# Kernel tuning notes

Hardware: AMD Instinct MI355X
Metric: run time of the kernel (lower is better)

The kernel has to match this reference:

```python
import jax, jax.numpy as jnp
from jax import lax
import numpy as np

BN_EPS = 1e-5

def nearest_resize(x, out_h, out_w):
    # torch F.interpolate(mode='nearest'): src = floor(dst * in / out)
    B, C, H, W = x.shape
    hi = (jnp.arange(out_h) * H) // out_h
    wi = (jnp.arange(out_w) * W) // out_w
    return x[:, :, hi][:, :, :, wi]

def conv1x1(x, w, b=None):
    y = jnp.einsum('bchw,oc->bohw', x, w)
    if b is not None:
        y = y + b[None, :, None, None]
    return y

def dwconv(x, w, stride, pad):
    C = x.shape[1]
    return lax.conv_general_dilated(x, w, (stride, stride), [(pad, pad), (pad, pad)],
                                    dimension_numbers=('NCHW', 'OIHW', 'NCHW'),
                                    feature_group_count=C)

def bn(x, g, b, m, v):
    scale = g / jnp.sqrt(v + BN_EPS)
    return (x - m[None, :, None, None]) * scale[None, :, None, None] + b[None, :, None, None]


def setup_inputs() -> dict:
    key = jax.random.key(0)
    ks = jax.random.split(key, 8)
    B, C, H0, W0 = 4, 512, 192, 192
    w_scale = 0.05
    return {
        'x': jax.random.normal(ks[0], (B, C, H0, W0), jnp.float32),
        'q_w': jax.random.normal(ks[1], (C, C), jnp.float32) * w_scale,
        'q_b': jnp.zeros((C,), jnp.float32),
        'kv_w': jax.random.normal(ks[2], (2 * C, C), jnp.float32) * w_scale,
        'kv_b': jnp.zeros((2 * C,), jnp.float32),
        'sr1_w': jax.random.normal(ks[3], (C, 1, 2, 2), jnp.float32) * w_scale,
        'bn1_g': jnp.ones((C,), jnp.float32),
        'bn1_b': jnp.zeros((C,), jnp.float32),
        'bn1_m': jnp.zeros((C,), jnp.float32),
        'bn1_v': jnp.ones((C,), jnp.float32),
        'sr2_w': jax.random.normal(ks[4], (C, C), jnp.float32) * w_scale,
        'bn2_g': jnp.ones((C,), jnp.float32),
        'bn2_b': jnp.zeros((C,), jnp.float32),
        'bn2_m': jnp.zeros((C,), jnp.float32),
        'bn2_v': jnp.ones((C,), jnp.float32),
        'lc_w': jax.random.normal(ks[5], (C, 1, 3, 3), jnp.float32) * w_scale,
        'lc_b': jnp.zeros((C,), jnp.float32),
        'head_num': 8,
    }


def reference(x, q_w, q_b, kv_w, kv_b, sr1_w, bn1_g, bn1_b, bn1_m, bn1_v,
              sr2_w, bn2_g, bn2_b, bn2_m, bn2_v, lc_w, lc_b, head_num):
    origin_h, origin_w = x.shape[2], x.shape[3]
    x = nearest_resize(x, origin_h // 4, origin_w // 4)
    B, C, H, W = x.shape
    hd = C // head_num
    scale = hd ** (-0.5)

    # q projection (1x1 conv with bias)
    q = conv1x1(x, q_w, q_b)  # [B,C,H,W]

    # spatial reduction: depthwise conv(k=sr, s=sr, p=sr//2) + BN + ReLU, then 1x1 + BN
    sr = sr1_w.shape[-1]
    kv = jax.nn.relu(bn(dwconv(x, sr1_w, sr, sr // 2), bn1_g, bn1_b, bn1_m, bn1_v))
    kv = bn(conv1x1(kv, sr2_w), bn2_g, bn2_b, bn2_m, bn2_v)

    # local depthwise 3x3 conv residual
    kv = dwconv(kv, lc_w, 1, 1) + lc_b[None, :, None, None] + kv

    # kv projection (1x1 conv, 2C output)
    kv = conv1x1(kv, kv_w, kv_b)
    k, v = jnp.split(kv, 2, axis=1)  # each [B,C,Hs,Ws]
    M = k.shape[2] * k.shape[3]

    q_ = jnp.swapaxes(q.reshape(B, head_num, hd, H * W), -1, -2)  # [B,h,N,hd]
    k_ = k.reshape(B, head_num, hd, M)                             # [B,h,hd,M]
    v_ = jnp.swapaxes(v.reshape(B, head_num, hd, M), -1, -2)       # [B,h,M,hd]

    attn = jax.nn.softmax(jnp.matmul(q_, k_) * scale, axis=-1)     # [B,h,N,M]
    out = jnp.swapaxes(jnp.matmul(attn, v_), -1, -2).reshape(B, C, H, W)

    # NOTE: original torch code passes size=(origin_w, origin_h)
    out = nearest_resize(out, origin_w, origin_h)
    return out
```

## Files before the change

### kernel.cpp

```cpp
#include <hip/hip_runtime.h>

#define Bsz 4
#define Cc  512
#define C2  1024
#define H0c 192
#define Hh  48
#define Nn  2304
#define HNh 8
#define HD  64
#define Hs  25
#define Ms  625

typedef const float* fp;
typedef _Float16 f16;
typedef __attribute__((ext_vector_type(8))) _Float16 f16x8;
typedef __attribute__((ext_vector_type(4))) _Float16 f16x4;
typedef __attribute__((ext_vector_type(4))) float    f32x4;

__global__ __launch_bounds__(256) void k_ds_t(fp __restrict__ x,
                                              float* __restrict__ xds,
                                              f16* __restrict__ xt) {
    __shared__ float tile[32][33];
    const int b = blockIdx.z;
    const int s0 = blockIdx.x * 32, r0 = blockIdx.y * 32;
    const int t = threadIdx.x;
    const float* xb = x + (size_t)b * Cc * H0c * H0c;
    float* xdsb = xds + (size_t)b * Cc * Nn;
    #pragma unroll
    for (int p = 0; p < 4; p++) {
        int e = t + p * 256; int i = e >> 5, j = e & 31;
        int c = r0 + i, n = s0 + j;
        float v = xb[((size_t)c * H0c + (n / Hh) * 4) * H0c + (n % Hh) * 4];
        tile[i][j] = v;
        xdsb[(size_t)c * Nn + n] = v;
    }
    __syncthreads();
    #pragma unroll
    for (int p = 0; p < 4; p++) {
        int e = t + p * 256; int oi = e >> 5, oj = e & 31;
        xt[((size_t)b * Nn + s0 + oi) * Cc + r0 + oj] = (f16)tile[oj][oi];
    }
}

__global__ __launch_bounds__(256) void k_sr1t(const float* __restrict__ xds,
                                              fp __restrict__ w, fp g, fp bb, fp bm, fp bv,
                                              f16* __restrict__ kv1t) {
    __shared__ float tile[32][33];
    const int b = blockIdx.z;
    const int s0 = blockIdx.x * 32, r0 = blockIdx.y * 32;
    const int t = threadIdx.x;
    #pragma unroll
    for (int p = 0; p < 4; p++) {
        int e = t + p * 256; int i = e >> 5, j = e & 31;
        int c = r0 + i, n = s0 + j;
        float v = 0.f;
        if (n < Ms) {
            int ho = n / Hs, wo = n % Hs;
            const float* src = xds + ((size_t)b * Cc + c) * Nn;
            float acc = 0.f;
            #pragma unroll
            for (int di = 0; di < 2; di++) {
                int ih = ho * 2 - 1 + di;
                if (ih < 0 || ih >= Hh) continue;
                #pragma unroll
                for (int dj = 0; dj < 2; dj++) {
                    int iw = wo * 2 - 1 + dj;
                    if (iw < 0 || iw >= Hh) continue;
                    acc += w[c * 4 + di * 2 + dj] * src[ih * Hh + iw];
                }
            }
            float sc = g[c] * rsqrtf(bv[c] + 1e-5f);
            v = fmaxf((acc - bm[c]) * sc + bb[c], 0.f);
        }
        tile[i][j] = v;
    }
    __syncthreads();
    #pragma unroll
    for (int p = 0; p < 4; p++) {
        int e = t + p * 256; int oi = e >> 5, oj = e & 31;
        if (s0 + oi < Ms)
            kv1t[((size_t)b * Ms + s0 + oi) * Cc + r0 + oj] = (f16)tile[oj][oi];
    }
}

__global__ __launch_bounds__(256) void k_lct(const float* __restrict__ kv2,
                                             fp __restrict__ w, fp __restrict__ lb,
                                             f16* __restrict__ kv3t) {
    __shared__ float tile[32][33];
    const int b = blockIdx.z;
    const int s0 = blockIdx.x * 32, r0 = blockIdx.y * 32;
    const int t = threadIdx.x;
    #pragma unroll
    for (int p = 0; p < 4; p++) {
        int e = t + p * 256; int i = e >> 5, j = e & 31;
        int c = r0 + i, n = s0 + j;
        float v = 0.f;
        if (n < Ms) {
            int ho = n / Hs, wo = n % Hs;
            const float* src = kv2 + ((size_t)b * Cc + c) * Ms;
            float acc = 0.f;
            #pragma unroll
            for (int di = 0; di < 3; di++) {
                int ih = ho - 1 + di;
                if (ih < 0 || ih >= Hs) continue;
                #pragma unroll
                for (int dj = 0; dj < 3; dj++) {
                    int iw = wo - 1 + dj;
                    if (iw < 0 || iw >= Hs) continue;
                    acc += w[c * 9 + di * 3 + dj] * src[ih * Hs + iw];
                }
            }
            v = acc + lb[c] + src[n];
        }
        tile[i][j] = v;
    }
    __syncthreads();
    #pragma unroll
    for (int p = 0; p < 4; p++) {
        int e = t + p * 256; int oi = e >> 5, oj = e & 31;
        if (s0 + oi < Ms)
            kv3t[((size_t)b * Ms + s0 + oi) * Cc + r0 + oj] = (f16)tile[oj][oi];
    }
}

__global__ __launch_bounds__(256) void k_gemm_mfma(
    const float* __restrict__ W, const f16* __restrict__ Xt,
    float* __restrict__ Yf, f16* __restrict__ Yt, f16* __restrict__ Vt,
    const int Md, const int Nd, const int NtRows, const int mode,
    fp __restrict__ bias,
    fp __restrict__ bn_g, fp __restrict__ bn_b, fp __restrict__ bn_m, fp __restrict__ bn_v)
{
    __shared__ f16 sA[128 * 80];
    __shared__ f16 sB[128 * 80];
    const int b  = blockIdx.z;
    const int m0 = blockIdx.y * 128, n0 = blockIdx.x * 128;
    const int t = threadIdx.x;
    const int lane = t & 63, w = t >> 6;
    const int lm = lane & 15, q = lane >> 4;
    const int wm = w >> 1, wn = w & 1;
    const f16* Xb = Xt + (size_t)b * Nd * 512;

    f32x4 acc[4][4];
    #pragma unroll
    for (int i = 0; i < 4; i++)
        #pragma unroll
        for (int j = 0; j < 4; j++)
            #pragma unroll
            for (int r = 0; r < 4; r++) acc[i][j][r] = 0.f;

    for (int k0 = 0; k0 < 512; k0 += 64) {
        {
            int r = t >> 1, hh = (t & 1) * 32;
            const float* wr = W + (size_t)(m0 + r) * 512 + k0 + hh;
            f16* dst = &sA[r * 80 + hh];
            #pragma unroll
            for (int i = 0; i < 8; i++) {
                float4 v = *(const float4*)&wr[i * 4];
                f16x4 h4; h4[0] = (f16)v.x; h4[1] = (f16)v.y; h4[2] = (f16)v.z; h4[3] = (f16)v.w;
                *(f16x4*)&dst[i * 4] = h4;
            }
        }
        {
            int r = t >> 1, hh = (t & 1) * 32;
            bool ok = (n0 + r) < Nd;
            const f16* xr = Xb + (size_t)(n0 + r) * 512 + k0 + hh;
            f16* dst = &sB[r * 80 + hh];
            #pragma unroll
            for (int i = 0; i < 4; i++) {
                f16x8 v;
                if (ok) {
                    v = *(const f16x8*)&xr[i * 8];
                } else {
                    for (int z = 0; z < 8; z++) v[z] = (f16)0.f;
                }
                *(f16x8*)&dst[i * 8] = v;
            }
        }
        __syncthreads();
        #pragma unroll
        for (int ks = 0; ks < 2; ks++) {
            f16x8 af[4], bf[4];
            #pragma unroll
            for (int i = 0; i < 4; i++)
                af[i] = *(const f16x8*)&sA[(wm * 64 + i * 16 + lm) * 80 + ks * 32 + q * 8];
            #pragma unroll
            for (int j = 0; j < 4; j++)
                bf[j] = *(const f16x8*)&sB[(wn * 64 + j * 16 + lm) * 80 + ks * 32 + q * 8];
            #pragma unroll
            for (int i = 0; i < 4; i++)
                #pragma unroll
                for (int j = 0; j < 4; j++)
                    acc[i][j] = __builtin_amdgcn_mfma_f32_16x16x32_f16(af[i], bf[j], acc[i][j], 0, 0, 0);
        }
        __syncthreads();
    }

    #pragma unroll
    for (int i = 0; i < 4; i++) {
        int ob = m0 + wm * 64 + i * 16 + q * 4;
        float badd[4], bsc[4], bsh[4];
        #pragma unroll
        for (int r = 0; r < 4; r++) {
            int o = ob + r;
            badd[r] = bias ? bias[o] : 0.f;
            if (bn_g) { bsc[r] = bn_g[o] * rsqrtf(bn_v[o] + 1e-5f); bsh[r] = bn_b[o] - bn_m[o] * bsc[r]; }
            else      { bsc[r] = 1.f; bsh[r] = 0.f; }
        }
        #pragma unroll
        for (int j = 0; j < 4; j++) {
            int n = n0 + wn * 64 + j * 16 + lm;
            f32x4 a = acc[i][j];
            if (mode == 0) {
                if (n < Nd) {
                    #pragma unroll
                    for (int r = 0; r < 4; r++)
                        Yf[((size_t)b * Md + ob + r) * Nd + n] = (a[r] + badd[r]) * bsc[r] + bsh[r];
                }
            } else if (mode == 1 || (mode == 2 && ob < 512)) {
                f16x4 h;
                #pragma unroll
                for (int r = 0; r < 4; r++) h[r] = (f16)(a[r] + badd[r]);
                int hh = ob >> 6, d0 = ob & 63;
                *(f16x4*)&Yt[((size_t)(b * 8 + hh) * NtRows + n) * 64 + d0] = h;
            } else {
                #pragma unroll
                for (int r = 0; r < 4; r++) {
                    float val = (n < Nd) ? (a[r] + badd[r]) : 0.f;
                    Vt[((size_t)b * Cc + (ob + r - 512)) * 640 + n] = (f16)val;
                }
            }
        }
    }
}

__global__ __launch_bounds__(256) void k_attn_mfma(
    const f16* __restrict__ Qt, const f16* __restrict__ Kt,
    const f16* __restrict__ Vt, float* __restrict__ out)
{
    __shared__ f16 sK[64 * 80];
    __shared__ f16 sV[64 * 80];
    __shared__ f16 sP[4][16 * 80];

    int bh = blockIdx.y;
    int n0 = blockIdx.x * 64;
    int t = threadIdx.x, w = t >> 6, lane = t & 63;
    int lm = lane & 15, q = lane >> 4;
    f16* sPw = &sP[w][0];

    f16x8 qf[2];
    {
        const f16* qrow = Qt + ((size_t)bh * Nn + n0 + w * 16 + lm) * 64;
        qf[0] = *(const f16x8*)&qrow[q * 8];
        qf[1] = *(const f16x8*)&qrow[32 + q * 8];
    }

    f32x4 od[4];
    #pragma unroll
    for (int dt = 0; dt < 4; dt++)
        #pragma unroll
        for (int r = 0; r < 4; r++) od[dt][r] = 0.f;
    float mold[4], lold[4];
    #pragma unroll
    for (int r = 0; r < 4; r++) { mold[r] = -1e30f; lold[r] = 0.f; }

    int kr = t >> 2, kc = t & 3;
    const f16* kbase = Kt + (size_t)bh * 640 * 64;
    const f16* vbase = Vt + (size_t)bh * 64 * 640;

    for (int mc = 0; mc < 640; mc += 64) {
        {
            const f16* ksrc = kbase + (size_t)(mc + kr) * 64;
            *(f16x8*)&sK[kr * 80 + kc * 8]      = *(const f16x8*)&ksrc[kc * 8];
            *(f16x8*)&sK[kr * 80 + 32 + kc * 8] = *(const f16x8*)&ksrc[32 + kc * 8];
            const f16* vsrc = vbase + (size_t)kr * 640 + mc;
            *(f16x8*)&sV[kr * 80 + kc * 8]      = *(const f16x8*)&vsrc[kc * 8];
            *(f16x8*)&sV[kr * 80 + 32 + kc * 8] = *(const f16x8*)&vsrc[32 + kc * 8];
        }
        __syncthreads();

        f32x4 sc4[4];
        #pragma unroll
        for (int j = 0; j < 4; j++)
            #pragma unroll
            for (int r = 0; r < 4; r++) sc4[j][r] = 0.f;
        #pragma unroll
        for (int ks = 0; ks < 2; ks++) {
            #pragma unroll
            for (int j = 0; j < 4; j++) {
                f16x8 kf = *(const f16x8*)&sK[(j * 16 + lm) * 80 + ks * 32 + q * 8];
                sc4[j] = __builtin_amdgcn_mfma_f32_16x16x32_f16(qf[ks], kf, sc4[j], 0, 0, 0);
            }
        }

        #pragma unroll
        for (int reg = 0; reg < 4; reg++) {
            float mx = -1e30f;
            #pragma unroll
            for (int j = 0; j < 4; j++) {
                float s = sc4[j][reg] * 0.125f;
                if (mc + j * 16 + lm >= Ms) s = -1e30f;
                sc4[j][reg] = s;
                mx = fmaxf(mx, s);
            }
            #pragma unroll
            for (int off = 1; off < 16; off <<= 1) mx = fmaxf(mx, __shfl_xor(mx, off));
            float mnew = fmaxf(mold[reg], mx);
            float alpha = __expf(mold[reg] - mnew);
            float rs = 0.f;
            #pragma unroll
            for (int j = 0; j < 4; j++) {
                float p = __expf(sc4[j][reg] - mnew);
                sc4[j][reg] = p;
                rs += p;
            }
            #pragma unroll
            for (int off = 1; off < 16; off <<= 1) rs += __shfl_xor(rs, off);
            lold[reg] = lold[reg] * alpha + rs;
            mold[reg] = mnew;
            #pragma unroll
            for (int dt = 0; dt < 4; dt++) od[dt][reg] *= alpha;
            #pragma unroll
            for (int j = 0; j < 4; j++)
                sPw[(q * 4 + reg) * 80 + j * 16 + lm] = (f16)sc4[j][reg];
        }

        #pragma unroll
        for (int ks = 0; ks < 2; ks++) {
            f16x8 pa = *(const f16x8*)&sPw[lm * 80 + ks * 32 + q * 8];
            #pragma unroll
            for (int dt = 0; dt < 4; dt++) {
                f16x8 vf = *(const f16x8*)&sV[(dt * 16 + lm) * 80 + ks * 32 + q * 8];
                od[dt] = __builtin_amdgcn_mfma_f32_16x16x32_f16(pa, vf, od[dt], 0, 0, 0);
            }
        }
        __syncthreads();
    }

    float inv4[4];
    #pragma unroll
    for (int r = 0; r < 4; r++) inv4[r] = 1.f / lold[r];
    const int bq = bh >> 3, hch = (bh & 7) * 64;
    const int nq = n0 + w * 16 + q * 4;
    const int i4 = (nq / Hh) * 4, j4 = (nq % Hh) * 4;
    #pragma unroll
    for (int dt = 0; dt < 4; dt++) {
        float* oc = out + ((size_t)(bq * Cc + hch + dt * 16 + lm) * H0c + i4) * H0c + j4;
        #pragma unroll
        for (int r = 0; r < 4; r++) {
            float val = od[dt][r] * inv4[r];
            float4 pk = make_float4(val, val, val, val);
            #pragma unroll
            for (int ii = 0; ii < 4; ii++)
                *(float4*)&oc[ii * H0c + r * 4] = pk;
        }
    }
}

extern "C" void kernel_launch(void* const* d_in, const int* in_sizes, int n_in,
                              void* d_out, int out_size, void* d_ws, size_t ws_size,
                              hipStream_t stream) {
    (void)in_sizes; (void)n_in; (void)out_size; (void)ws_size;
    fp x     = (fp)d_in[0];
    fp q_w   = (fp)d_in[1];
    fp q_b   = (fp)d_in[2];
    fp kv_w  = (fp)d_in[3];
    fp kv_b  = (fp)d_in[4];
    fp sr1_w = (fp)d_in[5];
    fp bn1_g = (fp)d_in[6];
    fp bn1_b = (fp)d_in[7];
    fp bn1_m = (fp)d_in[8];
    fp bn1_v = (fp)d_in[9];
    fp sr2_w = (fp)d_in[10];
    fp bn2_g = (fp)d_in[11];
    fp bn2_b = (fp)d_in[12];
    fp bn2_m = (fp)d_in[13];
    fp bn2_v = (fp)d_in[14];
    fp lc_w  = (fp)d_in[15];
    fp lc_b  = (fp)d_in[16];
    float* out = (float*)d_out;

    float* ws   = (float*)d_ws;
    float* xds  = ws;
    float* kv2  = ws;
    f16*   Kt   = (f16*)(ws + 1310720);
    f16*   vt   = (f16*)(ws + 1966080);
    f16*   xt   = (f16*)(ws + 4718592);
    f16*   kv1t = (f16*)(ws + 4718592);
    f16*   kv3t = (f16*)(ws + 5358592);
    f16*   Qt   = (f16*)(ws + 7077888);

    k_ds_t<<<dim3(72, 16, Bsz), 256, 0, stream>>>(x, xds, xt);
    k_gemm_mfma<<<dim3(18, 4, Bsz), 256, 0, stream>>>(q_w, xt, nullptr, Qt, nullptr,
        Cc, Nn, Nn, 1, q_b, nullptr, nullptr, nullptr, nullptr);
    k_sr1t<<<dim3(20, 16, Bsz), 256, 0, stream>>>(xds, sr1_w, bn1_g, bn1_b, bn1_m, bn1_v, kv1t);
    k_gemm_mfma<<<dim3(5, 4, Bsz), 256, 0, stream>>>(sr2_w, kv1t, kv2, nullptr, nullptr,
        Cc, Ms, 0, 0, nullptr, bn2_g, bn2_b, bn2_m, bn2_v);
    k_lct<<<dim3(20, 16, Bsz), 256, 0, stream>>>(kv2, lc_w, lc_b, kv3t);
    k_gemm_mfma<<<dim3(5, 8, Bsz), 256, 0, stream>>>(kv_w, kv3t, nullptr, Kt, vt,
        C2, Ms, 640, 2, kv_b, nullptr, nullptr, nullptr, nullptr);
    k_attn_mfma<<<dim3(Nn / 64, Bsz * HNh), 256, 0, stream>>>(Qt, Kt, vt, out);
}
```

Before: 690.5 us.

## Pre-convert weights to fp16, fold softmax scale into Q, split upsample into separate kernel

Adds a kernel that converts all three 1x1 weight matrices to fp16 once, so the GEMM loads fp16 weights directly instead of converting fp32 in every tile. The softmax scale is folded into the Q projection epilogue, and masking in attention is limited to the last key chunk. The attention kernel now writes a compact [B*C, N] buffer, and a new coalesced upsample kernel expands it to the full-resolution output. This replaces the strided 16x replicated stores from the attention epilogue, at the cost of extra launches and an extra intermediate round trip through memory.

```diff
diff --git a/kernel.cpp b/kernel.cpp
--- a/kernel.cpp
+++ b/kernel.cpp
@@ -17,6 +17,16 @@
 typedef __attribute__((ext_vector_type(4))) _Float16 f16x4;
 typedef __attribute__((ext_vector_type(4))) float    f32x4;
 
+__global__ __launch_bounds__(256) void k_cvtw(fp __restrict__ q_w, fp __restrict__ sr2_w,
+                                              fp __restrict__ kv_w, f16* __restrict__ wh) {
+    int idx = blockIdx.x * 256 + threadIdx.x;
+    float v;
+    if (idx < 262144)      v = q_w[idx];
+    else if (idx < 524288) v = sr2_w[idx - 262144];
+    else                   v = kv_w[idx - 524288];
+    wh[idx] = (f16)v;
+}
+
 __global__ __launch_bounds__(256) void k_ds_t(fp __restrict__ x,
                                               float* __restrict__ xds,
                                               f16* __restrict__ xt) {
@@ -124,9 +134,9 @@
 }
 
 __global__ __launch_bounds__(256) void k_gemm_mfma(
-    const float* __restrict__ W, const f16* __restrict__ Xt,
+    const f16* __restrict__ W, const f16* __restrict__ Xt,
     float* __restrict__ Yf, f16* __restrict__ Yt, f16* __restrict__ Vt,
-    const int Md, const int Nd, const int NtRows, const int mode,
+    const int Md, const int Nd, const int NtRows, const int mode, const float oscale,
     fp __restrict__ bias,
     fp __restrict__ bn_g, fp __restrict__ bn_b, fp __restrict__ bn_m, fp __restrict__ bn_v)
 {
@@ -151,14 +161,11 @@
     for (int k0 = 0; k0 < 512; k0 += 64) {
         {
             int r = t >> 1, hh = (t & 1) * 32;
-            const float* wr = W + (size_t)(m0 + r) * 512 + k0 + hh;
+            const f16* wr = W + (size_t)(m0 + r) * 512 + k0 + hh;
             f16* dst = &sA[r * 80 + hh];
             #pragma unroll
-            for (int i = 0; i < 8; i++) {
-                float4 v = *(const float4*)&wr[i * 4];
-                f16x4 h4; h4[0] = (f16)v.x; h4[1] = (f16)v.y; h4[2] = (f16)v.z; h4[3] = (f16)v.w;
-                *(f16x4*)&dst[i * 4] = h4;
-            }
+            for (int i = 0; i < 4; i++)
+                *(f16x8*)&dst[i * 8] = *(const f16x8*)&wr[i * 8];
         }
         {
             int r = t >> 1, hh = (t & 1) * 32;
@@ -219,7 +226,7 @@
             } else if (mode == 1 || (mode == 2 && ob < 512)) {
                 f16x4 h;
                 #pragma unroll
-                for (int r = 0; r < 4; r++) h[r] = (f16)(a[r] + badd[r]);
+                for (int r = 0; r < 4; r++) h[r] = (f16)((a[r] + badd[r]) * oscale);
                 int hh = ob >> 6, d0 = ob & 63;
                 *(f16x4*)&Yt[((size_t)(b * 8 + hh) * NtRows + n) * 64 + d0] = h;
             } else {
@@ -235,7 +242,7 @@
 
 __global__ __launch_bounds__(256) void k_attn_mfma(
     const f16* __restrict__ Qt, const f16* __restrict__ Kt,
-    const f16* __restrict__ Vt, float* __restrict__ out)
+    const f16* __restrict__ Vt, float* __restrict__ Obuf)
 {
     __shared__ f16 sK[64 * 80];
     __shared__ f16 sV[64 * 80];
@@ -292,15 +299,22 @@
             }
         }
 
+        const bool lastc = (mc >= 576);
         #pragma unroll
         for (int reg = 0; reg < 4; reg++) {
-            float mx = -1e30f;
-            #pragma unroll
-            for (int j = 0; j < 4; j++) {
-                float s = sc4[j][reg] * 0.125f;
-                if (mc + j * 16 + lm >= Ms) s = -1e30f;
-                sc4[j][reg] = s;
-                mx = fmaxf(mx, s);
+            float mx;
+            if (lastc) {
+                mx = -1e30f;
+                #pragma unroll
+                for (int j = 0; j < 4; j++) {
+                    float s = sc4[j][reg];
+                    if (576 + j * 16 + lm >= Ms) s = -1e30f;
+                    sc4[j][reg] = s;
+                    mx = fmaxf(mx, s);
+                }
+            } else {
+                mx = fmaxf(fmaxf(sc4[0][reg], sc4[1][reg]),
+                           fmaxf(sc4[2][reg], sc4[3][reg]));
             }
             #pragma unroll
             for (int off = 1; off < 16; off <<= 1) mx = fmaxf(mx, __shfl_xor(mx, off));
@@ -336,24 +350,29 @@
         __syncthreads();
     }
 
-    float inv4[4];
-    #pragma unroll
-    for (int r = 0; r < 4; r++) inv4[r] = 1.f / lold[r];
-    const int bq = bh >> 3, hch = (bh & 7) * 64;
-    const int nq = n0 + w * 16 + q * 4;
-    const int i4 = (nq / Hh) * 4, j4 = (nq % Hh) * 4;
+    float inv[4];
+    #pragma unroll
+    for (int r = 0; r < 4; r++) inv[r] = 1.f / lold[r];
     #pragma unroll
     for (int dt = 0; dt < 4; dt++) {
-        float* oc = out + ((size_t)(bq * Cc + hch + dt * 16 + lm) * H0c + i4) * H0c + j4;
-        #pragma unroll
-        for (int r = 0; r < 4; r++) {
-            float val = od[dt][r] * inv4[r];
-            float4 pk = make_float4(val, val, val, val);
-            #pragma unroll
-            for (int ii = 0; ii < 4; ii++)
-                *(float4*)&oc[ii * H0c + r * 4] = pk;
-        }
-    }
+        f32x4 o;
+        #pragma unroll
+        for (int r = 0; r < 4; r++) o[r] = od[dt][r] * inv[r];
+        size_t c = (size_t)bh * 64 + dt * 16 + lm;
+        *(f32x4*)&Obuf[c * Nn + n0 + w * 16 + q * 4] = o;
+    }
+}
+
+__global__ __launch_bounds__(256) void k_upsample(const float* __restrict__ O,
+                                                  float* __restrict__ out) {
+    size_t idx = (size_t)blockIdx.x * 256 + threadIdx.x;
+    if (idx >= (size_t)Bsz * Cc * H0c * 48) return;
+    int jg = (int)(idx % 48);
+    int i  = (int)((idx / 48) % H0c);
+    int bc = (int)(idx / ((size_t)48 * H0c));
+    float s = O[(size_t)bc * Nn + (i >> 2) * Hh + jg];
+    float4 pack = make_float4(s, s, s, s);
+    *(float4*)(out + ((size_t)bc * H0c + i) * H0c + jg * 4) = pack;
 }
 
 extern "C" void kernel_launch(void* const* d_in, const int* in_sizes, int n_in,
@@ -381,22 +400,26 @@
 
     float* ws   = (float*)d_ws;
     float* xds  = ws;
-    float* kv2  = ws;
-    f16*   Kt   = (f16*)(ws + 1310720);
-    f16*   vt   = (f16*)(ws + 1966080);
-    f16*   xt   = (f16*)(ws + 4718592);
-    f16*   kv1t = (f16*)(ws + 4718592);
-    f16*   kv3t = (f16*)(ws + 5358592);
-    f16*   Qt   = (f16*)(ws + 7077888);
-
+    float* Obuf = ws;
+    float* kv2  = ws + 4718592;
+    f16*   Kt   = (f16*)(ws + 5998592);
+    f16*   vt   = (f16*)(ws + 6653952);
+    f16*   xt   = (f16*)(ws + 7309312);
+    f16*   kv1t = xt;
+    f16*   kv3t = xt;
+    f16*   Qt   = (f16*)(ws + 9668608);
+    f16*   wh   = (f16*)(ws + 12027904);
+
+    k_cvtw<<<4096, 256, 0, stream>>>(q_w, sr2_w, kv_w, wh);
     k_ds_t<<<dim3(72, 16, Bsz), 256, 0, stream>>>(x, xds, xt);
-    k_gemm_mfma<<<dim3(18, 4, Bsz), 256, 0, stream>>>(q_w, xt, nullptr, Qt, nullptr,
-        Cc, Nn, Nn, 1, q_b, nullptr, nullptr, nullptr, nullptr);
+    k_gemm_mfma<<<dim3(18, 4, Bsz), 256, 0, stream>>>(wh, xt, nullptr, Qt, nullptr,
+        Cc, Nn, Nn, 1, 0.125f, q_b, nullptr, nullptr, nullptr, nullptr);
     k_sr1t<<<dim3(20, 16, Bsz), 256, 0, stream>>>(xds, sr1_w, bn1_g, bn1_b, bn1_m, bn1_v, kv1t);
-    k_gemm_mfma<<<dim3(5, 4, Bsz), 256, 0, stream>>>(sr2_w, kv1t, kv2, nullptr, nullptr,
-        Cc, Ms, 0, 0, nullptr, bn2_g, bn2_b, bn2_m, bn2_v);
+    k_gemm_mfma<<<dim3(5, 4, Bsz), 256, 0, stream>>>(wh + 262144, kv1t, kv2, nullptr, nullptr,
+        Cc, Ms, 0, 0, 1.f, nullptr, bn2_g, bn2_b, bn2_m, bn2_v);
     k_lct<<<dim3(20, 16, Bsz), 256, 0, stream>>>(kv2, lc_w, lc_b, kv3t);
-    k_gemm_mfma<<<dim3(5, 8, Bsz), 256, 0, stream>>>(kv_w, kv3t, nullptr, Kt, vt,
-        C2, Ms, 640, 2, kv_b, nullptr, nullptr, nullptr, nullptr);
-    k_attn_mfma<<<dim3(Nn / 64, Bsz * HNh), 256, 0, stream>>>(Qt, Kt, vt, out);
-}
+    k_gemm_mfma<<<dim3(5, 8, Bsz), 256, 0, stream>>>(wh + 524288, kv3t, nullptr, Kt, vt,
+        C2, Ms, 640, 2, 1.f, kv_b, nullptr, nullptr, nullptr, nullptr);
+    k_attn_mfma<<<dim3(Nn / 64, Bsz * HNh), 256, 0, stream>>>(Qt, Kt, vt, Obuf);
+    k_upsample<<<(unsigned)((size_t)Bsz * Cc * H0c * 48 / 256), 256, 0, stream>>>(Obuf, out);
+}
```

Measured after the change: 617.2 us. 1.12x faster.
